# Kernel tuning notes

Hardware: AMD Instinct MI355X
Metric: run time of the kernel (lower is better)

## Reference

```python
import jax, jax.numpy as jnp
import numpy as np

NUM_CLUSTERS = 8
DIM_IN, DIM_HID = 1024, 256
N = 65536


def setup_inputs() -> dict:
    key = jax.random.key(0)
    ks = jax.random.split(key, 12)
    s_in = 1.0 / np.sqrt(DIM_IN)
    s_h = 1.0 / np.sqrt(DIM_HID)
    return {
        "x_path": jax.random.normal(ks[0], (1, N, DIM_IN), dtype=jnp.float32),
        "cluster_id": jax.random.randint(ks[1], (N,), 0, NUM_CLUSTERS),
        "W1": jax.random.normal(ks[2], (DIM_HID, DIM_IN), dtype=jnp.float32) * s_in,
        "b1": jax.random.normal(ks[3], (DIM_HID,), dtype=jnp.float32) * s_in,
        "Wf": jax.random.normal(ks[4], (DIM_HID, DIM_HID), dtype=jnp.float32) * s_h,
        "bf": jax.random.normal(ks[5], (DIM_HID,), dtype=jnp.float32) * s_h,
        "Wa": jax.random.normal(ks[6], (DIM_HID, DIM_HID), dtype=jnp.float32) * s_h,
        "ba": jax.random.normal(ks[7], (DIM_HID,), dtype=jnp.float32) * s_h,
        "Wb": jax.random.normal(ks[8], (DIM_HID, DIM_HID), dtype=jnp.float32) * s_h,
        "bb": jax.random.normal(ks[9], (DIM_HID,), dtype=jnp.float32) * s_h,
        "Wc": jax.random.normal(ks[10], (1, DIM_HID), dtype=jnp.float32) * s_h,
        "bc": jax.random.normal(ks[11], (1,), dtype=jnp.float32) * s_h,
    }


def reference(x_path, cluster_id, W1, b1, Wf, bf, Wa, ba, Wb, bb, Wc, bc):
    x = x_path[0]  # [N, dim_in]
    # per-instance 1x1 conv + ReLU (== linear + ReLU)
    h = jax.nn.relu(jnp.einsum('nd,hd->nh', x, W1) + b1)  # [N, dim_hid]
    # segment mean over clusters (AdaptiveAvgPool1d(1) per cluster); empty -> 0
    seg_sum = jax.ops.segment_sum(h, cluster_id, num_segments=NUM_CLUSTERS)
    counts = jax.ops.segment_sum(jnp.ones((h.shape[0],), h.dtype), cluster_id,
                                 num_segments=NUM_CLUSTERS)
    h_cluster = seg_sum / jnp.maximum(counts, 1.0)[:, None]  # [K, dim_hid]
    # attention net: Linear + ReLU (dropout is inference identity)
    h_path = jax.nn.relu(h_cluster @ Wf.T + bf)  # [K, dim_hid]
    # gated attention (CLAM Attn_Net_Gated)
    a = jnp.tanh(h_path @ Wa.T + ba)
    g = jax.nn.sigmoid(h_path @ Wb.T + bb)
    A = (a * g) @ Wc.T + bc            # [K, 1]
    A = jax.nn.softmax(A.T, axis=1)    # [1, K]
    H = A @ h_path                     # [1, dim_hid]
    return H
```

## Files before the change

### kernel.cpp

```cpp
#include <hip/hip_runtime.h>
#include <hip/hip_bf16.h>

#define NN    65536
#define KDIM  1024
#define HDIM  256
#define NC    8
#define BM    64
#define NKB   16

typedef __bf16 bf16x8 __attribute__((ext_vector_type(8)));
typedef float  f32x4  __attribute__((ext_vector_type(4)));
typedef __attribute__((address_space(1))) void GV;
typedef __attribute__((address_space(3))) void LV;

static __device__ __forceinline__ void async_cp16(const void* g, void* l) {
    __builtin_amdgcn_global_load_lds((GV*)g, (LV*)l, 16, 0, 0);
}

static __device__ __forceinline__ unsigned short f2bf_rne(float f) {
    unsigned int u = __float_as_uint(f);
    unsigned int r = u + 0x7fffu + ((u >> 16) & 1u);
    return (unsigned short)(r >> 16);
}

static __device__ __forceinline__ unsigned long long pack4bf(float4 v) {
    return (unsigned long long)f2bf_rne(v.x)
         | ((unsigned long long)f2bf_rne(v.y) << 16)
         | ((unsigned long long)f2bf_rne(v.z) << 32)
         | ((unsigned long long)f2bf_rne(v.w) << 48);
}

__global__ __launch_bounds__(256) void prep_kernel(
    const float* __restrict__ W1, unsigned short* __restrict__ W1b,
    const int* __restrict__ cid, int* __restrict__ cnt_partial)
{
    __shared__ int hcnt[NC];
    if (threadIdx.x < NC) hcnt[threadIdx.x] = 0;
    __syncthreads();

    const int gid = blockIdx.x * 256 + threadIdx.x;
    const int kc  = gid & 3;
    const int n   = (gid >> 2) & 255;
    const int h   = (gid >> 10) & 1;
    const int kbi = gid >> 11;
    const float* src = W1 + (size_t)n * KDIM + kbi * 64 + h * 32 + kc * 8;
    float4 v0 = *(const float4*)(src);
    float4 v1 = *(const float4*)(src + 4);
    ulonglong2 pk;
    pk.x = pack4bf(v0);
    pk.y = pack4bf(v1);
    *(ulonglong2*)(W1b + (size_t)gid * 8) = pk;

    atomicAdd(&hcnt[cid[gid]], 1);
    atomicAdd(&hcnt[cid[gid + 32768]], 1);
    __syncthreads();
    if (threadIdx.x < NC)
        cnt_partial[blockIdx.x * NC + threadIdx.x] = hcnt[threadIdx.x];
}

__global__ __launch_bounds__(256, 3) void gemm_kernel(
    const float* __restrict__ x, const int* __restrict__ cid,
    const unsigned short* __restrict__ W1b, const float* __restrict__ b1,
    float* __restrict__ partial)
{
    __shared__ __align__(16) unsigned short xs[2][BM * 32];
    __shared__ __align__(16) unsigned short wsb[2][HDIM * 32];
    __shared__ float lsums[HDIM * NC];
    __shared__ int cids[BM];

    const int tid  = threadIdx.x;
    const int wave = tid >> 6;
    const int lane = tid & 63;
    const int l15  = lane & 15;
    const int q    = lane >> 4;
    const int row0 = blockIdx.x * BM;

    for (int i = tid; i < HDIM * NC; i += 256) lsums[i] = 0.0f;
    if (tid < BM) cids[tid] = cid[row0 + tid];

    f32x4 acc[4][4];
    #pragma unroll
    for (int i = 0; i < 4; ++i)
        #pragma unroll
        for (int j = 0; j < 4; ++j)
            #pragma unroll
            for (int r = 0; r < 4; ++r) acc[i][j][r] = 0.0f;

    const unsigned short* wg0 = W1b + ((size_t)(wave * 512 + lane)) * 8;
    unsigned short* wl0 = &wsb[0][0] + wave * 4096;

    const int xr = tid >> 4, xc = tid & 15;
    const float* xg = x + (size_t)(row0 + xr) * KDIM + xc * 4;

    float4 nx[4];
    #pragma unroll
    for (int p = 0; p < 4; ++p)
        nx[p] = *(const float4*)(xg + (size_t)p * 16 * KDIM);

    for (int kbi = 0; kbi < NKB; ++kbi) {
        __syncthreads();

        #pragma unroll
        for (int p = 0; p < 4; ++p) {
            unsigned long long pk = pack4bf(nx[p]);
            int r = p * 16 + xr;
            *(unsigned long long*)&xs[xc >> 3][r * 32 + (xc & 7) * 4] = pk;
        }
        const unsigned short* wg = wg0 + (size_t)kbi * 16384;
        #pragma unroll
        for (int t = 0; t < 8; ++t)
            async_cp16(wg + t * 512, wl0 + t * 512);

        __syncthreads();

        if (kbi < NKB - 1) {
            #pragma unroll
            for (int p = 0; p < 4; ++p)
                nx[p] = *(const float4*)(xg + (kbi + 1) * 64 + (size_t)p * 16 * KDIM);
        }

        #pragma unroll
        for (int s = 0; s < 2; ++s) {
            bf16x8 af[4], bfr[4];
            #pragma unroll
            for (int i = 0; i < 4; ++i)
                af[i] = *(const bf16x8*)&xs[s][(i * 16 + l15) * 32 + q * 8];
            #pragma unroll
            for (int j = 0; j < 4; ++j)
                bfr[j] = *(const bf16x8*)&wsb[s][(wave * 64 + j * 16 + l15) * 32 + q * 8];
            #pragma unroll
            for (int i = 0; i < 4; ++i)
                #pragma unroll
                for (int j = 0; j < 4; ++j)
                    acc[i][j] = __builtin_amdgcn_mfma_f32_16x16x32_bf16(af[i], bfr[j], acc[i][j], 0, 0, 0);
        }
    }

    float b1v[4];
    #pragma unroll
    for (int j = 0; j < 4; ++j) b1v[j] = b1[wave * 64 + j * 16 + l15];

    #pragma unroll
    for (int i = 0; i < 4; ++i) {
        #pragma unroll
        for (int j = 0; j < 4; ++j) {
            const int col = wave * 64 + j * 16 + l15;
            #pragma unroll
            for (int r = 0; r < 4; ++r) {
                float v = fmaxf(acc[i][j][r] + b1v[j], 0.0f);
                int m = i * 16 + q * 4 + r;
                atomicAdd(&lsums[col * NC + cids[m]], v);
            }
        }
    }
    __syncthreads();
    float* dst = partial + (size_t)blockIdx.x * 2048 + tid * 8;
    *(f32x4*)dst       = *(const f32x4*)&lsums[tid * 8];
    *(f32x4*)(dst + 4) = *(const f32x4*)&lsums[tid * 8 + 4];
}

__global__ __launch_bounds__(256) void reduce_kernel(
    const float* __restrict__ partial, float* __restrict__ stage2)
{
    const int s  = blockIdx.x >> 3;
    const int og = blockIdx.x & 7;
    const int o  = og * 256 + threadIdx.x;
    const float* p = partial + (size_t)s * 128 * 2048 + o;
    float a0=0,a1=0,a2=0,a3=0,a4=0,a5=0,a6=0,a7=0;
    #pragma unroll 4
    for (int pb = 0; pb < 128; pb += 8) {
        a0 += p[(size_t)(pb+0)*2048]; a1 += p[(size_t)(pb+1)*2048];
        a2 += p[(size_t)(pb+2)*2048]; a3 += p[(size_t)(pb+3)*2048];
        a4 += p[(size_t)(pb+4)*2048]; a5 += p[(size_t)(pb+5)*2048];
        a6 += p[(size_t)(pb+6)*2048]; a7 += p[(size_t)(pb+7)*2048];
    }
    stage2[(size_t)s * 2048 + o] = ((a0+a1)+(a2+a3)) + ((a4+a5)+(a6+a7));
}

__global__ __launch_bounds__(256) void head_kernel(
    const float* __restrict__ stage2, const int* __restrict__ cnt_partial,
    const float* __restrict__ Wf, const float* __restrict__ bf1,
    const float* __restrict__ Wa, const float* __restrict__ ba,
    const float* __restrict__ Wb, const float* __restrict__ bb,
    const float* __restrict__ Wc, const float* __restrict__ bc,
    float* __restrict__ out)
{
    __shared__ float hcT[HDIM * NC];
    __shared__ float hpT[HDIM * NC];
    __shared__ float red[NC * 4];
    __shared__ int   cnt_s[256];
    __shared__ float cnt_f[NC];
    const int c = threadIdx.x;
    const int wave = c >> 6, lane = c & 63;

    {
        int k = c & 7, g = c >> 3;
        const int* cp = cnt_partial + g * 32 + k;
        cnt_s[c] = cp[0] + cp[8] + cp[16] + cp[24];
    }
    __syncthreads();
    if (c < NC) {
        int s = 0;
        #pragma unroll
        for (int g = 0; g < 32; ++g) s += cnt_s[g * 8 + c];
        cnt_f[c] = 1.0f / fmaxf((float)s, 1.0f);
    }
    __syncthreads();

    {
        float a[NC] = {0,0,0,0,0,0,0,0};
        #pragma unroll
        for (int s = 0; s < 8; ++s) {
            f32x4 u0 = *(const f32x4*)&stage2[(size_t)s * 2048 + c * 8];
            f32x4 u1 = *(const f32x4*)&stage2[(size_t)s * 2048 + c * 8 + 4];
            a[0]+=u0[0]; a[1]+=u0[1]; a[2]+=u0[2]; a[3]+=u0[3];
            a[4]+=u1[0]; a[5]+=u1[1]; a[6]+=u1[2]; a[7]+=u1[3];
        }
        #pragma unroll
        for (int k = 0; k < NC; ++k) hcT[c * NC + k] = a[k] * cnt_f[k];
    }
    __syncthreads();

    {
        float acc[NC];
        float bias = bf1[c];
        #pragma unroll
        for (int k = 0; k < NC; ++k) acc[k] = bias;
        const float4* wf4 = (const float4*)(Wf + (size_t)c * HDIM);
        for (int d4 = 0; d4 < 64; ++d4) {
            float4 w = wf4[d4];
            #pragma unroll
            for (int e = 0; e < 4; ++e) {
                float wd = (e == 0) ? w.x : (e == 1) ? w.y : (e == 2) ? w.z : w.w;
                const f32x4 h0 = *(const f32x4*)&hcT[(d4 * 4 + e) * NC];
                const f32x4 h1 = *(const f32x4*)&hcT[(d4 * 4 + e) * NC + 4];
                acc[0] += wd * h0[0]; acc[1] += wd * h0[1];
                acc[2] += wd * h0[2]; acc[3] += wd * h0[3];
                acc[4] += wd * h1[0]; acc[5] += wd * h1[1];
                acc[6] += wd * h1[2]; acc[7] += wd * h1[3];
            }
        }
        #pragma unroll
        for (int k = 0; k < NC; ++k) hpT[c * NC + k] = fmaxf(acc[k], 0.0f);
    }
    __syncthreads();

    float za[NC], zb[NC];
    {
        float biasa = ba[c], biasb = bb[c];
        #pragma unroll
        for (int k = 0; k < NC; ++k) { za[k] = biasa; zb[k] = biasb; }
        const float4* wa4 = (const float4*)(Wa + (size_t)c * HDIM);
        const float4* wb4 = (const float4*)(Wb + (size_t)c * HDIM);
        for (int d4 = 0; d4 < 64; ++d4) {
            float4 wa = wa4[d4], wb = wb4[d4];
            #pragma unroll
            for (int e = 0; e < 4; ++e) {
                float wav = (e == 0) ? wa.x : (e == 1) ? wa.y : (e == 2) ? wa.z : wa.w;
                float wbv = (e == 0) ? wb.x : (e == 1) ? wb.y : (e == 2) ? wb.z : wb.w;
                const f32x4 h0 = *(const f32x4*)&hpT[(d4 * 4 + e) * NC];
                const f32x4 h1 = *(const f32x4*)&hpT[(d4 * 4 + e) * NC + 4];
                za[0] += wav * h0[0]; za[1] += wav * h0[1]; za[2] += wav * h0[2]; za[3] += wav * h0[3];
                za[4] += wav * h1[0]; za[5] += wav * h1[1]; za[6] += wav * h1[2]; za[7] += wav * h1[3];
                zb[0] += wbv * h0[0]; zb[1] += wbv * h0[1]; zb[2] += wbv * h0[2]; zb[3] += wbv * h0[3];
                zb[4] += wbv * h1[0]; zb[5] += wbv * h1[1]; zb[6] += wbv * h1[2]; zb[7] += wbv * h1[3];
            }
        }
    }
    float wcv = Wc[c];
    float v[NC];
    #pragma unroll
    for (int k = 0; k < NC; ++k) {
        float a = tanhf(za[k]);
        float g = 1.0f / (1.0f + expf(-zb[k]));
        v[k] = a * g * wcv;
    }
    #pragma unroll
    for (int k = 0; k < NC; ++k) {
        float s = v[k];
        #pragma unroll
        for (int off = 32; off > 0; off >>= 1) s += __shfl_down(s, off, 64);
        if (lane == 0) red[k * 4 + wave] = s;
    }
    __syncthreads();
    float logit[NC], m = -1e30f;
    #pragma unroll
    for (int k = 0; k < NC; ++k) {
        logit[k] = red[k * 4] + red[k * 4 + 1] + red[k * 4 + 2] + red[k * 4 + 3] + bc[0];
        m = fmaxf(m, logit[k]);
    }
    float s = 0.0f, ex[NC];
    #pragma unroll
    for (int k = 0; k < NC; ++k) { ex[k] = expf(logit[k] - m); s += ex[k]; }
    float inv = 1.0f / s;
    float o = 0.0f;
    #pragma unroll
    for (int k = 0; k < NC; ++k) o += ex[k] * inv * hpT[c * NC + k];
    out[c] = o;
}

extern "C" void kernel_launch(void* const* d_in, const int* in_sizes, int n_in,
                              void* d_out, int out_size, void* d_ws, size_t ws_size,
                              hipStream_t stream)
{
    (void)in_sizes; (void)n_in; (void)out_size; (void)ws_size;
    const float* x   = (const float*)d_in[0];
    const int*   cid = (const int*)  d_in[1];
    const float* W1  = (const float*)d_in[2];
    const float* b1  = (const float*)d_in[3];
    const float* Wf  = (const float*)d_in[4];
    const float* bfv = (const float*)d_in[5];
    const float* Wa  = (const float*)d_in[6];
    const float* ba  = (const float*)d_in[7];
    const float* Wb  = (const float*)d_in[8];
    const float* bb  = (const float*)d_in[9];
    const float* Wc  = (const float*)d_in[10];
    const float* bc  = (const float*)d_in[11];
    float* out = (float*)d_out;

    unsigned short* W1b   = (unsigned short*)d_ws;
    int*   cnt_partial    = (int*)  ((char*)d_ws + 524288);
    float* partial        = (float*)((char*)d_ws + 528384);
    float* stage2         = (float*)((char*)d_ws + 528384 + 8388608);

    hipLaunchKernelGGL(prep_kernel,   dim3(128),     dim3(256), 0, stream, W1, W1b, cid, cnt_partial);
    hipLaunchKernelGGL(gemm_kernel,   dim3(NN / BM), dim3(256), 0, stream, x, cid, W1b, b1, partial);
    hipLaunchKernelGGL(reduce_kernel, dim3(64),      dim3(256), 0, stream, partial, stage2);
    hipLaunchKernelGGL(head_kernel,   dim3(1),       dim3(256), 0, stream,
                       stage2, cnt_partial, Wf, bfv, Wa, ba, Wb, bb, Wc, bc, out);
}
```

Measured before the change: 534.3 us.

## Load x directly into MFMA fragments and double-buffer W1 with async LDS copies

Each lane now loads its x values straight from global memory into registers in MFMA fragment layout and converts them to bf16 in registers, so the x tile no longer passes through LDS. W1 tiles are double-buffered in LDS with K-steps of 32, and the next tile is prefetched asynchronously. A single vmcnt wait plus one barrier per step replaces the two barriers per step. This targets LDS traffic and synchronisation stalls in the memory-bound GEMM. In exchange there are twice as many loop iterations and the lane-strided x loads are less coalesced, and correctness depends on the hand-encoded waitcnt value.

After: 628.4 us. 17.6% more time.

```diff
diff --git a/kernel.cpp b/kernel.cpp
--- a/kernel.cpp
+++ b/kernel.cpp
@@ -6,7 +6,7 @@
 #define HDIM  256
 #define NC    8
 #define BM    64
-#define NKB   16
+#define NKB2  32
 
 typedef __bf16 bf16x8 __attribute__((ext_vector_type(8)));
 typedef float  f32x4  __attribute__((ext_vector_type(4)));
@@ -16,6 +16,8 @@
 static __device__ __forceinline__ void async_cp16(const void* g, void* l) {
     __builtin_amdgcn_global_load_lds((GV*)g, (LV*)l, 16, 0, 0);
 }
+
+#define WAIT_VM8() __builtin_amdgcn_s_waitcnt(0x0F78)
 
 static __device__ __forceinline__ unsigned short f2bf_rne(float f) {
     unsigned int u = __float_as_uint(f);
@@ -30,6 +32,16 @@
          | ((unsigned long long)f2bf_rne(v.w) << 48);
 }
 
+static __device__ __forceinline__ bf16x8 cvt8(float4 a, float4 b) {
+    __hip_bfloat162 p0 = __float22bfloat162_rn(float2{a.x, a.y});
+    __hip_bfloat162 p1 = __float22bfloat162_rn(float2{a.z, a.w});
+    __hip_bfloat162 p2 = __float22bfloat162_rn(float2{b.x, b.y});
+    __hip_bfloat162 p3 = __float22bfloat162_rn(float2{b.z, b.w});
+    union { __hip_bfloat162 h[4]; bf16x8 v; } u;
+    u.h[0] = p0; u.h[1] = p1; u.h[2] = p2; u.h[3] = p3;
+    return u.v;
+}
+
 __global__ __launch_bounds__(256) void prep_kernel(
     const float* __restrict__ W1, unsigned short* __restrict__ W1b,
     const int* __restrict__ cid, int* __restrict__ cnt_partial)
@@ -41,9 +53,8 @@
     const int gid = blockIdx.x * 256 + threadIdx.x;
     const int kc  = gid & 3;
     const int n   = (gid >> 2) & 255;
-    const int h   = (gid >> 10) & 1;
-    const int kbi = gid >> 11;
-    const float* src = W1 + (size_t)n * KDIM + kbi * 64 + h * 32 + kc * 8;
+    const int kb2 = gid >> 10;
+    const float* src = W1 + (size_t)n * KDIM + kb2 * 32 + kc * 8;
     float4 v0 = *(const float4*)(src);
     float4 v1 = *(const float4*)(src + 4);
     ulonglong2 pk;
@@ -63,8 +74,7 @@
     const unsigned short* __restrict__ W1b, const float* __restrict__ b1,
     float* __restrict__ partial)
 {
-    __shared__ __align__(16) unsigned short xs[2][BM * 32];
-    __shared__ __align__(16) unsigned short wsb[2][HDIM * 32];
+    __shared__ __align__(16) unsigned short wsb[2][1024 * 8];
     __shared__ float lsums[HDIM * NC];
     __shared__ int cids[BM];
 
@@ -77,6 +87,7 @@
 
     for (int i = tid; i < HDIM * NC; i += 256) lsums[i] = 0.0f;
     if (tid < BM) cids[tid] = cid[row0 + tid];
+    __syncthreads();
 
     f32x4 acc[4][4];
     #pragma unroll
@@ -86,53 +97,64 @@
             #pragma unroll
             for (int r = 0; r < 4; ++r) acc[i][j][r] = 0.0f;
 
-    const unsigned short* wg0 = W1b + ((size_t)(wave * 512 + lane)) * 8;
-    unsigned short* wl0 = &wsb[0][0] + wave * 4096;
-
-    const int xr = tid >> 4, xc = tid & 15;
-    const float* xg = x + (size_t)(row0 + xr) * KDIM + xc * 4;
-
-    float4 nx[4];
-    #pragma unroll
-    for (int p = 0; p < 4; ++p)
-        nx[p] = *(const float4*)(xg + (size_t)p * 16 * KDIM);
-
-    for (int kbi = 0; kbi < NKB; ++kbi) {
-        __syncthreads();
-
-        #pragma unroll
-        for (int p = 0; p < 4; ++p) {
-            unsigned long long pk = pack4bf(nx[p]);
-            int r = p * 16 + xr;
-            *(unsigned long long*)&xs[xc >> 3][r * 32 + (xc & 7) * 4] = pk;
-        }
-        const unsigned short* wg = wg0 + (size_t)kbi * 16384;
-        #pragma unroll
-        for (int t = 0; t < 8; ++t)
-            async_cp16(wg + t * 512, wl0 + t * 512);
-
-        __syncthreads();
-
-        if (kbi < NKB - 1) {
-            #pragma unroll
-            for (int p = 0; p < 4; ++p)
-                nx[p] = *(const float4*)(xg + (kbi + 1) * 64 + (size_t)p * 16 * KDIM);
-        }
-
-        #pragma unroll
-        for (int s = 0; s < 2; ++s) {
-            bf16x8 af[4], bfr[4];
-            #pragma unroll
-            for (int i = 0; i < 4; ++i)
-                af[i] = *(const bf16x8*)&xs[s][(i * 16 + l15) * 32 + q * 8];
+    const unsigned short* wgl = W1b + (size_t)(wave * 256 + lane) * 8;
+
+    const float* xb0 = x + (size_t)(row0 + 0 * 16 + l15) * KDIM + q * 8;
+    const float* xb1 = x + (size_t)(row0 + 1 * 16 + l15) * KDIM + q * 8;
+    const float* xb2 = x + (size_t)(row0 + 2 * 16 + l15) * KDIM + q * 8;
+    const float* xb3 = x + (size_t)(row0 + 3 * 16 + l15) * KDIM + q * 8;
+
+    float4 xf[8];
+
+    {
+        unsigned short* wl = (unsigned short*)&wsb[0][0] + wave * 2048;
+        #pragma unroll
+        for (int t = 0; t < 4; ++t)
+            async_cp16(wgl + t * 512, wl + t * 512);
+        xf[0] = *(const float4*)(xb0);  xf[1] = *(const float4*)(xb0 + 4);
+        xf[2] = *(const float4*)(xb1);  xf[3] = *(const float4*)(xb1 + 4);
+        xf[4] = *(const float4*)(xb2);  xf[5] = *(const float4*)(xb2 + 4);
+        xf[6] = *(const float4*)(xb3);  xf[7] = *(const float4*)(xb3 + 4);
+        WAIT_VM8();
+        __builtin_amdgcn_s_barrier();
+    }
+
+    for (int kb = 0; kb < NKB2; ++kb) {
+        const int cur = kb & 1;
+
+        bf16x8 af[4];
+        af[0] = cvt8(xf[0], xf[1]);
+        af[1] = cvt8(xf[2], xf[3]);
+        af[2] = cvt8(xf[4], xf[5]);
+        af[3] = cvt8(xf[6], xf[7]);
+
+        if (kb + 1 < NKB2) {
+            unsigned short* wl = (unsigned short*)&wsb[cur ^ 1][0] + wave * 2048;
+            const unsigned short* wg = wgl + (size_t)(kb + 1) * 8192;
+            #pragma unroll
+            for (int t = 0; t < 4; ++t)
+                async_cp16(wg + t * 512, wl + t * 512);
+            xb0 += 32; xb1 += 32; xb2 += 32; xb3 += 32;
+            xf[0] = *(const float4*)(xb0);  xf[1] = *(const float4*)(xb0 + 4);
+            xf[2] = *(const float4*)(xb1);  xf[3] = *(const float4*)(xb1 + 4);
+            xf[4] = *(const float4*)(xb2);  xf[5] = *(const float4*)(xb2 + 4);
+            xf[6] = *(const float4*)(xb3);  xf[7] = *(const float4*)(xb3 + 4);
+        }
+
+        bf16x8 bfr[4];
+        #pragma unroll
+        for (int j = 0; j < 4; ++j)
+            bfr[j] = *(const bf16x8*)&wsb[cur][((wave * 64 + j * 16 + l15) * 4 + q) * 8];
+
+        #pragma unroll
+        for (int i = 0; i < 4; ++i)
             #pragma unroll
             for (int j = 0; j < 4; ++j)
-                bfr[j] = *(const bf16x8*)&wsb[s][(wave * 64 + j * 16 + l15) * 32 + q * 8];
-            #pragma unroll
-            for (int i = 0; i < 4; ++i)
-                #pragma unroll
-                for (int j = 0; j < 4; ++j)
-                    acc[i][j] = __builtin_amdgcn_mfma_f32_16x16x32_bf16(af[i], bfr[j], acc[i][j], 0, 0, 0);
+                acc[i][j] = __builtin_amdgcn_mfma_f32_16x16x32_bf16(af[i], bfr[j], acc[i][j], 0, 0, 0);
+
+        if (kb + 1 < NKB2) {
+            WAIT_VM8();
+            __builtin_amdgcn_s_barrier();
         }
     }
 
```

## Restructure GEMM pipeline: async fp32 x to LDS, register-resident W1 fragments, triple buffering

Applied to the files above, without the earlier changes.

The main loop is rebuilt around a triple-buffered LDS ring. Fp32 x tiles are copied asynchronously with global_load_lds into XOR-swizzled LDS and converted to bf16 at fragment-read time. Pre-packed W1 fragments (prep now lays them out in MFMA fragment order) are loaded straight into double-buffered registers instead of going through LDS. Manual waitcnt and barrier calls replace the two __syncthreads per step, and occupancy is raised from 3 to 4 blocks per CU. This aims to hide global-load latency and cut LDS traffic and sync overhead, at the risk of fragile hand-coded waitcnt values and more register pressure.

New measurement: 524.3 us. About the same (-1.9%).

```diff
diff --git a/kernel.cpp b/kernel.cpp
--- a/kernel.cpp
+++ b/kernel.cpp
@@ -6,7 +6,7 @@
 #define HDIM  256
 #define NC    8
 #define BM    64
-#define NKB   16
+#define NPH   32
 
 typedef __bf16 bf16x8 __attribute__((ext_vector_type(8)));
 typedef float  f32x4  __attribute__((ext_vector_type(4)));
@@ -16,6 +16,11 @@
 static __device__ __forceinline__ void async_cp16(const void* g, void* l) {
     __builtin_amdgcn_global_load_lds((GV*)g, (LV*)l, 16, 0, 0);
 }
+
+#define WAIT_VM6()        __builtin_amdgcn_s_waitcnt(0x0F76)
+#define WAIT_VM4()        __builtin_amdgcn_s_waitcnt(0x0F74)
+#define WAIT_VM6_LGKM0()  __builtin_amdgcn_s_waitcnt(0x0076)
+#define SCHED_PIN()       __builtin_amdgcn_sched_barrier(0)
 
 static __device__ __forceinline__ unsigned short f2bf_rne(float f) {
     unsigned int u = __float_as_uint(f);
@@ -30,6 +35,16 @@
          | ((unsigned long long)f2bf_rne(v.w) << 48);
 }
 
+static __device__ __forceinline__ bf16x8 cvt8(f32x4 a, f32x4 b) {
+    __hip_bfloat162 p0 = __float22bfloat162_rn(float2{a[0], a[1]});
+    __hip_bfloat162 p1 = __float22bfloat162_rn(float2{a[2], a[3]});
+    __hip_bfloat162 p2 = __float22bfloat162_rn(float2{b[0], b[1]});
+    __hip_bfloat162 p3 = __float22bfloat162_rn(float2{b[2], b[3]});
+    union { __hip_bfloat162 h[4]; bf16x8 v; } u;
+    u.h[0] = p0; u.h[1] = p1; u.h[2] = p2; u.h[3] = p3;
+    return u.v;
+}
+
 __global__ __launch_bounds__(256) void prep_kernel(
     const float* __restrict__ W1, unsigned short* __restrict__ W1b,
     const int* __restrict__ cid, int* __restrict__ cnt_partial)
@@ -38,12 +53,14 @@
     if (threadIdx.x < NC) hcnt[threadIdx.x] = 0;
     __syncthreads();
 
-    const int gid = blockIdx.x * 256 + threadIdx.x;
-    const int kc  = gid & 3;
-    const int n   = (gid >> 2) & 255;
-    const int h   = (gid >> 10) & 1;
-    const int kbi = gid >> 11;
-    const float* src = W1 + (size_t)n * KDIM + kbi * 64 + h * 32 + kc * 8;
+    const int gid  = blockIdx.x * 256 + threadIdx.x;
+    const int lane = gid & 63;
+    const int j    = (gid >> 6) & 3;
+    const int wv   = (gid >> 8) & 3;
+    const int kb   = gid >> 10;
+    const int n    = wv * 64 + j * 16 + (lane & 15);
+    const int k0   = kb * 32 + (lane >> 4) * 8;
+    const float* src = W1 + (size_t)n * KDIM + k0;
     float4 v0 = *(const float4*)(src);
     float4 v1 = *(const float4*)(src + 4);
     ulonglong2 pk;
@@ -58,13 +75,12 @@
         cnt_partial[blockIdx.x * NC + threadIdx.x] = hcnt[threadIdx.x];
 }
 
-__global__ __launch_bounds__(256, 3) void gemm_kernel(
+__global__ __launch_bounds__(256, 4) void gemm_kernel(
     const float* __restrict__ x, const int* __restrict__ cid,
     const unsigned short* __restrict__ W1b, const float* __restrict__ b1,
     float* __restrict__ partial)
 {
-    __shared__ __align__(16) unsigned short xs[2][BM * 32];
-    __shared__ __align__(16) unsigned short wsb[2][HDIM * 32];
+    __shared__ __align__(16) char xs[3 * 8192];
     __shared__ float lsums[HDIM * NC];
     __shared__ int cids[BM];
 
@@ -78,6 +94,15 @@
     for (int i = tid; i < HDIM * NC; i += 256) lsums[i] = 0.0f;
     if (tid < BM) cids[tid] = cid[row0 + tid];
 
+    const int rl = lane >> 3;
+    const int cl = (lane & 7) ^ rl;
+    const float* xg = x + (size_t)(row0 + wave * 16 + rl) * KDIM + cl * 4;
+
+    const unsigned short* bg = W1b + (size_t)(wave * 256 + lane) * 8;
+
+    const int le0 = l15 * 128 + (((2 * q + 0) ^ (l15 & 7)) * 16);
+    const int le1 = l15 * 128 + (((2 * q + 1) ^ (l15 & 7)) * 16);
+
     f32x4 acc[4][4];
     #pragma unroll
     for (int i = 0; i < 4; ++i)
@@ -86,53 +111,64 @@
             #pragma unroll
             for (int r = 0; r < 4; ++r) acc[i][j][r] = 0.0f;
 
-    const unsigned short* wg0 = W1b + ((size_t)(wave * 512 + lane)) * 8;
-    unsigned short* wl0 = &wsb[0][0] + wave * 4096;
-
-    const int xr = tid >> 4, xc = tid & 15;
-    const float* xg = x + (size_t)(row0 + xr) * KDIM + xc * 4;
-
-    float4 nx[4];
-    #pragma unroll
-    for (int p = 0; p < 4; ++p)
-        nx[p] = *(const float4*)(xg + (size_t)p * 16 * KDIM);
-
-    for (int kbi = 0; kbi < NKB; ++kbi) {
-        __syncthreads();
-
-        #pragma unroll
-        for (int p = 0; p < 4; ++p) {
-            unsigned long long pk = pack4bf(nx[p]);
-            int r = p * 16 + xr;
-            *(unsigned long long*)&xs[xc >> 3][r * 32 + (xc & 7) * 4] = pk;
-        }
-        const unsigned short* wg = wg0 + (size_t)kbi * 16384;
-        #pragma unroll
-        for (int t = 0; t < 8; ++t)
-            async_cp16(wg + t * 512, wl0 + t * 512);
-
-        __syncthreads();
-
-        if (kbi < NKB - 1) {
-            #pragma unroll
-            for (int p = 0; p < 4; ++p)
-                nx[p] = *(const float4*)(xg + (kbi + 1) * 64 + (size_t)p * 16 * KDIM);
-        }
-
-        #pragma unroll
-        for (int s = 0; s < 2; ++s) {
-            bf16x8 af[4], bfr[4];
-            #pragma unroll
-            for (int i = 0; i < 4; ++i)
-                af[i] = *(const bf16x8*)&xs[s][(i * 16 + l15) * 32 + q * 8];
+    bf16x8 bA[4], bB[4];
+
+    #pragma unroll
+    for (int h = 0; h < 2; ++h)
+        async_cp16(xg + (size_t)h * 8 * KDIM, &xs[wave * 2048 + h * 1024]);
+    #pragma unroll
+    for (int j = 0; j < 4; ++j)
+        bA[j] = *(const bf16x8*)(bg + j * 512);
+    #pragma unroll
+    for (int h = 0; h < 2; ++h)
+        async_cp16(xg + (size_t)h * 8 * KDIM + 32, &xs[8192 + wave * 2048 + h * 1024]);
+    SCHED_PIN();
+    WAIT_VM6_LGKM0();
+    __builtin_amdgcn_s_barrier();
+    SCHED_PIN();
+
+    #pragma unroll
+    for (int kb = 0; kb < NPH; ++kb) {
+        const int buf = kb % 3;
+        bf16x8* curB = (kb & 1) ? bB : bA;
+        bf16x8* nxtB = (kb & 1) ? bA : bB;
+
+        if (kb + 1 < NPH) {
             #pragma unroll
             for (int j = 0; j < 4; ++j)
-                bfr[j] = *(const bf16x8*)&wsb[s][(wave * 64 + j * 16 + l15) * 32 + q * 8];
-            #pragma unroll
-            for (int i = 0; i < 4; ++i)
-                #pragma unroll
-                for (int j = 0; j < 4; ++j)
-                    acc[i][j] = __builtin_amdgcn_mfma_f32_16x16x32_bf16(af[i], bfr[j], acc[i][j], 0, 0, 0);
+                nxtB[j] = *(const bf16x8*)(bg + (size_t)(kb + 1) * 8192 + j * 512);
+        }
+        if (kb + 2 < NPH) {
+            const int b2 = (kb + 2) % 3;
+            #pragma unroll
+            for (int h = 0; h < 2; ++h)
+                async_cp16(xg + (size_t)h * 8 * KDIM + (kb + 2) * 32,
+                           &xs[b2 * 8192 + wave * 2048 + h * 1024]);
+        }
+
+        bf16x8 af[4];
+        #pragma unroll
+        for (int i = 0; i < 4; ++i) {
+            const f32x4 v0 = *(const f32x4*)&xs[buf * 8192 + i * 2048 + le0];
+            const f32x4 v1 = *(const f32x4*)&xs[buf * 8192 + i * 2048 + le1];
+            af[i] = cvt8(v0, v1);
+        }
+        #pragma unroll
+        for (int i = 0; i < 4; ++i)
+            #pragma unroll
+            for (int j = 0; j < 4; ++j)
+                acc[i][j] = __builtin_amdgcn_mfma_f32_16x16x32_bf16(af[i], curB[j], acc[i][j], 0, 0, 0);
+
+        if (kb < NPH - 2) {
+            SCHED_PIN();
+            if (kb < NPH - 2 - 1 + 1 && kb + 2 < NPH) WAIT_VM6(); else WAIT_VM4();
+            __builtin_amdgcn_s_barrier();
+            SCHED_PIN();
+        } else if (kb == NPH - 2) {
+            SCHED_PIN();
+            WAIT_VM4();
+            __builtin_amdgcn_s_barrier();
+            SCHED_PIN();
         }
     }
 
```

## Pre-convert x to bf16 in MFMA fragment layout and drop LDS staging in GEMM

Applied to the files above, without the earlier changes.

A new convert kernel turns x from fp32 into bf16 and writes it in the exact per-lane fragment order the MFMA reads. W1 is repacked into the same fragment layout. The GEMM then loads A and B fragments straight from global memory into registers with a one-step software prefetch, so the LDS staging buffers and the barriers inside the loop go away. The cost is an extra full pass over x: a 256 MB fp32 read plus a 128 MB bf16 write before the GEMM reads the bf16 copy back. Each wave also now loads its B fragments from global memory on its own.

New measurement: 573.2 us. +7.3%, slower.

```diff
diff --git a/kernel.cpp b/kernel.cpp
--- a/kernel.cpp
+++ b/kernel.cpp
@@ -6,16 +6,10 @@
 #define HDIM  256
 #define NC    8
 #define BM    64
-#define NKB   16
+#define NPH   32
 
 typedef __bf16 bf16x8 __attribute__((ext_vector_type(8)));
 typedef float  f32x4  __attribute__((ext_vector_type(4)));
-typedef __attribute__((address_space(1))) void GV;
-typedef __attribute__((address_space(3))) void LV;
-
-static __device__ __forceinline__ void async_cp16(const void* g, void* l) {
-    __builtin_amdgcn_global_load_lds((GV*)g, (LV*)l, 16, 0, 0);
-}
 
 static __device__ __forceinline__ unsigned short f2bf_rne(float f) {
     unsigned int u = __float_as_uint(f);
@@ -30,6 +24,33 @@
          | ((unsigned long long)f2bf_rne(v.w) << 48);
 }
 
+__global__ __launch_bounds__(256) void convert_kernel(
+    const float* __restrict__ x, unsigned short* __restrict__ xb)
+{
+    __shared__ unsigned short tile[16 * 1032];
+    const int tid = threadIdx.x;
+    const int B0  = blockIdx.x;
+    const float* src = x + (size_t)B0 * 16 * KDIM;
+
+    #pragma unroll 4
+    for (int rep = 0; rep < 16; ++rep) {
+        float4 v = *(const float4*)(src + (size_t)rep * KDIM + tid * 4);
+        *(unsigned long long*)&tile[rep * 1032 + tid * 4] = pack4bf(v);
+    }
+    __syncthreads();
+
+    const int rb = B0 >> 2, ii = B0 & 3;
+    unsigned short* dstbase = xb + (size_t)rb * 65536 + ii * 512;
+    #pragma unroll
+    for (int wr = 0; wr < 8; ++wr) {
+        int g    = wr * 256 + tid;
+        int kb   = g >> 6, lane = g & 63;
+        int q    = lane >> 4, l15 = lane & 15;
+        ulonglong2 v = *(const ulonglong2*)&tile[l15 * 1032 + kb * 32 + q * 8];
+        *(ulonglong2*)(dstbase + (size_t)kb * 2048 + lane * 8) = v;
+    }
+}
+
 __global__ __launch_bounds__(256) void prep_kernel(
     const float* __restrict__ W1, unsigned short* __restrict__ W1b,
     const int* __restrict__ cid, int* __restrict__ cnt_partial)
@@ -38,12 +59,14 @@
     if (threadIdx.x < NC) hcnt[threadIdx.x] = 0;
     __syncthreads();
 
-    const int gid = blockIdx.x * 256 + threadIdx.x;
-    const int kc  = gid & 3;
-    const int n   = (gid >> 2) & 255;
-    const int h   = (gid >> 10) & 1;
-    const int kbi = gid >> 11;
-    const float* src = W1 + (size_t)n * KDIM + kbi * 64 + h * 32 + kc * 8;
+    const int gid  = blockIdx.x * 256 + threadIdx.x;
+    const int lane = gid & 63;
+    const int j    = (gid >> 6) & 3;
+    const int wv   = (gid >> 8) & 3;
+    const int kb   = gid >> 10;
+    const int n    = wv * 64 + j * 16 + (lane & 15);
+    const int k0   = kb * 32 + (lane >> 4) * 8;
+    const float* src = W1 + (size_t)n * KDIM + k0;
     float4 v0 = *(const float4*)(src);
     float4 v1 = *(const float4*)(src + 4);
     ulonglong2 pk;
@@ -59,12 +82,10 @@
 }
 
 __global__ __launch_bounds__(256, 3) void gemm_kernel(
-    const float* __restrict__ x, const int* __restrict__ cid,
+    const unsigned short* __restrict__ xb, const int* __restrict__ cid,
     const unsigned short* __restrict__ W1b, const float* __restrict__ b1,
     float* __restrict__ partial)
 {
-    __shared__ __align__(16) unsigned short xs[2][BM * 32];
-    __shared__ __align__(16) unsigned short wsb[2][HDIM * 32];
     __shared__ float lsums[HDIM * NC];
     __shared__ int cids[BM];
 
@@ -73,7 +94,8 @@
     const int lane = tid & 63;
     const int l15  = lane & 15;
     const int q    = lane >> 4;
-    const int row0 = blockIdx.x * BM;
+    const int rb   = blockIdx.x;
+    const int row0 = rb * BM;
 
     for (int i = tid; i < HDIM * NC; i += 256) lsums[i] = 0.0f;
     if (tid < BM) cids[tid] = cid[row0 + tid];
@@ -86,56 +108,36 @@
             #pragma unroll
             for (int r = 0; r < 4; ++r) acc[i][j][r] = 0.0f;
 
-    const unsigned short* wg0 = W1b + ((size_t)(wave * 512 + lane)) * 8;
-    unsigned short* wl0 = &wsb[0][0] + wave * 4096;
-
-    const int xr = tid >> 4, xc = tid & 15;
-    const float* xg = x + (size_t)(row0 + xr) * KDIM + xc * 4;
-
-    float4 nx[4];
-    #pragma unroll
-    for (int p = 0; p < 4; ++p)
-        nx[p] = *(const float4*)(xg + (size_t)p * 16 * KDIM);
-
-    for (int kbi = 0; kbi < NKB; ++kbi) {
-        __syncthreads();
-
-        #pragma unroll
-        for (int p = 0; p < 4; ++p) {
-            unsigned long long pk = pack4bf(nx[p]);
-            int r = p * 16 + xr;
-            *(unsigned long long*)&xs[xc >> 3][r * 32 + (xc & 7) * 4] = pk;
-        }
-        const unsigned short* wg = wg0 + (size_t)kbi * 16384;
-        #pragma unroll
-        for (int t = 0; t < 8; ++t)
-            async_cp16(wg + t * 512, wl0 + t * 512);
-
-        __syncthreads();
-
-        if (kbi < NKB - 1) {
-            #pragma unroll
-            for (int p = 0; p < 4; ++p)
-                nx[p] = *(const float4*)(xg + (kbi + 1) * 64 + (size_t)p * 16 * KDIM);
-        }
-
-        #pragma unroll
-        for (int s = 0; s < 2; ++s) {
-            bf16x8 af[4], bfr[4];
+    const unsigned short* ag = xb  + (size_t)rb * 65536 + lane * 8;
+    const unsigned short* bg = W1b + (size_t)wave * 2048 + lane * 8;
+
+    bf16x8 cA[4], cB[4];
+    #pragma unroll
+    for (int i = 0; i < 4; ++i) cA[i] = *(const bf16x8*)(ag + i * 512);
+    #pragma unroll
+    for (int j = 0; j < 4; ++j) cB[j] = *(const bf16x8*)(bg + j * 512);
+
+    #pragma unroll 2
+    for (int kb = 0; kb < NPH; ++kb) {
+        bf16x8 nA[4], nB[4];
+        if (kb + 1 < NPH) {
             #pragma unroll
             for (int i = 0; i < 4; ++i)
-                af[i] = *(const bf16x8*)&xs[s][(i * 16 + l15) * 32 + q * 8];
+                nA[i] = *(const bf16x8*)(ag + (size_t)(kb + 1) * 2048 + i * 512);
             #pragma unroll
             for (int j = 0; j < 4; ++j)
-                bfr[j] = *(const bf16x8*)&wsb[s][(wave * 64 + j * 16 + l15) * 32 + q * 8];
-            #pragma unroll
-            for (int i = 0; i < 4; ++i)
-                #pragma unroll
-                for (int j = 0; j < 4; ++j)
-                    acc[i][j] = __builtin_amdgcn_mfma_f32_16x16x32_bf16(af[i], bfr[j], acc[i][j], 0, 0, 0);
-        }
-    }
-
+                nB[j] = *(const bf16x8*)(bg + (size_t)(kb + 1) * 8192 + j * 512);
+        }
+        #pragma unroll
+        for (int i = 0; i < 4; ++i)
+            #pragma unroll
+            for (int j = 0; j < 4; ++j)
+                acc[i][j] = __builtin_amdgcn_mfma_f32_16x16x32_bf16(cA[i], cB[j], acc[i][j], 0, 0, 0);
+        #pragma unroll
+        for (int i = 0; i < 4; ++i) { cA[i] = nA[i]; cB[i] = nB[i]; }
+    }
+
+    __syncthreads();
     float b1v[4];
     #pragma unroll
     for (int j = 0; j < 4; ++j) b1v[j] = b1[wave * 64 + j * 16 + l15];
@@ -154,7 +156,7 @@
         }
     }
     __syncthreads();
-    float* dst = partial + (size_t)blockIdx.x * 2048 + tid * 8;
+    float* dst = partial + (size_t)rb * 2048 + tid * 8;
     *(f32x4*)dst       = *(const f32x4*)&lsums[tid * 8];
     *(f32x4*)(dst + 4) = *(const f32x4*)&lsums[tid * 8 + 4];
 }
@@ -320,12 +322,14 @@
 
     unsigned short* W1b   = (unsigned short*)d_ws;
     int*   cnt_partial    = (int*)  ((char*)d_ws + 524288);
-    float* partial        = (float*)((char*)d_ws + 528384);
-    float* stage2         = (float*)((char*)d_ws + 528384 + 8388608);
-
-    hipLaunchKernelGGL(prep_kernel,   dim3(128),     dim3(256), 0, stream, W1, W1b, cid, cnt_partial);
-    hipLaunchKernelGGL(gemm_kernel,   dim3(NN / BM), dim3(256), 0, stream, x, cid, W1b, b1, partial);
-    hipLaunchKernelGGL(reduce_kernel, dim3(64),      dim3(256), 0, stream, partial, stage2);
-    hipLaunchKernelGGL(head_kernel,   dim3(1),       dim3(256), 0, stream,
+    float* stage2         = (float*)((char*)d_ws + 528384);
+    float* partial        = (float*)((char*)d_ws + 593920);
+    unsigned short* xb    = (unsigned short*)((char*)d_ws + 8982528);
+
+    hipLaunchKernelGGL(convert_kernel, dim3(4096),    dim3(256), 0, stream, x, xb);
+    hipLaunchKernelGGL(prep_kernel,    dim3(128),     dim3(256), 0, stream, W1, W1b, cid, cnt_partial);
+    hipLaunchKernelGGL(gemm_kernel,    dim3(NN / BM), dim3(256), 0, stream, xb, cid, W1b, b1, partial);
+    hipLaunchKernelGGL(reduce_kernel,  dim3(64),      dim3(256), 0, stream, partial, stage2);
+    hipLaunchKernelGGL(head_kernel,    dim3(1),       dim3(256), 0, stream,
                        stage2, cnt_partial, Wf, bfv, Wa, ba, Wb, bb, Wc, bc, out);
 }
```
